# Kernel tuning notes

Hardware: AMD Instinct MI355X
Metric: run time of the kernel (lower is better)

The kernel has to match this reference:

```python
import jax, jax.numpy as jnp
import numpy as np

NA = 100000
NB = 100000
N_REL = 6
REL_SRC = ['A', 'B', 'A', 'B', 'A', 'B']
REL_DST = ['B', 'A', 'A', 'B', 'B', 'A']
N_NODES = {'A': NA, 'B': NB}
H_DIM, OUT_DIM, N_BASES, N_EDGES = 64, 16, 4, 500000


def setup_inputs() -> dict:
    key = jax.random.key(0)
    ks = jax.random.split(key, 16)
    inp = {
        'embed_A': jax.random.normal(ks[0], (NA, H_DIM), jnp.float32) * 0.1,
        'embed_B': jax.random.normal(ks[1], (NB, H_DIM), jnp.float32) * 0.1,
        'bias0': jnp.zeros((H_DIM,), jnp.float32),
        'w_comp1': jax.random.normal(ks[2], (N_REL, N_BASES), jnp.float32) * 0.5,
        'basis1': jax.random.normal(ks[3], (N_BASES, H_DIM, H_DIM), jnp.float32) * (1.0 / np.sqrt(H_DIM)),
        'bias1': jnp.zeros((H_DIM,), jnp.float32),
        'w_comp2': jax.random.normal(ks[4], (N_REL, N_BASES), jnp.float32) * 0.5,
        'basis2': jax.random.normal(ks[5], (N_BASES, H_DIM, OUT_DIM), jnp.float32) * (1.0 / np.sqrt(H_DIM)),
        'bias2': jnp.zeros((OUT_DIM,), jnp.float32),
    }
    for r in range(N_REL):
        inp[f'src_r{r}'] = jax.random.randint(ks[6 + r], (N_EDGES,), 0, N_NODES[REL_SRC[r]], jnp.int32)
        inp[f'dst_r{r}'] = jax.random.randint(jax.random.fold_in(ks[6 + r], 7), (N_EDGES,), 0, N_NODES[REL_DST[r]], jnp.int32)
    return inp


def _hetero_conv(h, W_rels, bias, edges, out_dim, activation):
    # h: dict ntype -> [N, d_in]; W_rels: None or [n_rel, d_in, d_out]
    out = {nt: jnp.zeros((N_NODES[nt], out_dim), h['A'].dtype) for nt in N_NODES}
    for r in range(N_REL):
        src_t, dst_t = REL_SRC[r], REL_DST[r]
        src, dst = edges[r]
        x = h[src_t] if W_rels is None else h[src_t] @ W_rels[r]  # [N_src, d_out]
        msg = x[src]  # gather: [E, d_out]
        n_dst = N_NODES[dst_t]
        agg = jax.ops.segment_sum(msg, dst, num_segments=n_dst)
        deg = jax.ops.segment_sum(jnp.ones((msg.shape[0],), msg.dtype), dst, num_segments=n_dst)
        out[dst_t] = out[dst_t] + agg / jnp.maximum(deg, 1.0)[:, None]  # norm='right'
    out = {nt: out[nt] + bias for nt in out}
    if activation is not None:
        out = {nt: activation(out[nt]) for nt in out}
    return out


def reference(embed_A, embed_B, bias0, w_comp1, basis1, bias1, w_comp2, basis2, bias2,
              src_r0, dst_r0, src_r1, dst_r1, src_r2, dst_r2,
              src_r3, dst_r3, src_r4, dst_r4, src_r5, dst_r5):
    edges = [(src_r0, dst_r0), (src_r1, dst_r1), (src_r2, dst_r2),
             (src_r3, dst_r3), (src_r4, dst_r4), (src_r5, dst_r5)]
    h = {'A': embed_A, 'B': embed_B}
    # layer 0: weight=False -> pure normalized aggregation + bias + relu
    h = _hetero_conv(h, None, bias0, edges, H_DIM, jax.nn.relu)
    # hidden layer with basis-decomposed weights
    W1 = jnp.einsum('rb,bio->rio', w_comp1, basis1)
    h = _hetero_conv(h, W1, bias1, edges, H_DIM, jax.nn.relu)
    # output layer, no activation
    W2 = jnp.einsum('rb,bio->rio', w_comp2, basis2)
    h = _hetero_conv(h, W2, bias2, edges, OUT_DIM, None)
    return h['A']  # logits for category node type
```

## Files before the change

### kernel.cpp

```cpp
#include <hip/hip_runtime.h>

#define NN 100000
#define EE 500000
#define DD 64
#define OD 16
#define NR 6
#define NBASE 4
#define BSH 10
#define NBK 98
#define SBLK 128
#define FLATN (NBK * SBLK)
#define STCAP 5632
#define DBIN 64
#define DBLK 128
#define FLAT2 (DBIN * DBLK)
#define NVR 8

struct Edges { const int* src[NR]; const int* dst[NR]; };

typedef __attribute__((ext_vector_type(8))) short bf16x8;
typedef __attribute__((ext_vector_type(4))) float f32x4;

__device__ __forceinline__ float bf2f(ushort u) {
    union { unsigned int i; float f; } v; v.i = ((unsigned int)u) << 16; return v.f;
}
__device__ __forceinline__ ushort f2bf(float f) {
    unsigned int x = __float_as_uint(f);
    unsigned int r = (x + 0x7fffu + ((x >> 16) & 1u)) >> 16;
    return (ushort)r;
}
__device__ __forceinline__ void bfpair(unsigned int u, float& lo, float& hi) {
    lo = __uint_as_float(u << 16);
    hi = __uint_as_float(u & 0xffff0000u);
}

__global__ __launch_bounds__(256) void build_w_kernel(
    const float* __restrict__ wc1, const float* __restrict__ b1,
    const float* __restrict__ wc2, const float* __restrict__ b2,
    ushort* __restrict__ Wp1, ushort* __restrict__ Wp2)
{
    int idx = blockIdx.x * blockDim.x + threadIdx.x;
    const int n1 = NR * DD * DD;
    const int n2 = NR * DD * OD;
    if (idx < n1) {
        int r = idx >> 12, rem = idx & 4095;
        int i = rem >> 6, o = rem & 63;
        float s = 0.f;
        #pragma unroll
        for (int b = 0; b < NBASE; ++b) s += wc1[r * NBASE + b] * b1[b * 4096 + rem];
        Wp1[(((size_t)(r * 8 + (i >> 3)) * 64 + o) << 3) + (i & 7)] = f2bf(s);
    } else if (idx < n1 + n2) {
        int j = idx - n1;
        int r = j >> 10, rem = j & 1023;
        int i = rem >> 4, o = rem & 15;
        float s = 0.f;
        #pragma unroll
        for (int b = 0; b < NBASE; ++b) s += wc2[r * NBASE + b] * b2[b * 1024 + rem];
        Wp2[(((size_t)(r * 8 + (i >> 3)) * 16 + o) << 3) + (i & 7)] = f2bf(s);
    }
}

__global__ __launch_bounds__(256) void cvt_kernel(
    const float* __restrict__ in, ushort* __restrict__ out, int n4)
{
    int i = blockIdx.x * 256 + threadIdx.x;
    if (i >= n4) return;
    float4 v = ((const float4*)in)[i];
    ushort4 o;
    o.x = f2bf(v.x); o.y = f2bf(v.y); o.z = f2bf(v.z); o.w = f2bf(v.w);
    ((ushort4*)out)[i] = o;
}

__global__ __launch_bounds__(256) void count_kernel(Edges ep, int* __restrict__ cnt_mat)
{
    __shared__ int h[NBK];
    int r = blockIdx.y, blk = blockIdx.x;
    const int* __restrict__ dst = ep.dst[r];
    const int chunk = (EE + SBLK - 1) / SBLK;
    int e0 = blk * chunk, e1 = min(e0 + chunk, EE);
    for (int i = threadIdx.x; i < NBK; i += 256) h[i] = 0;
    __syncthreads();
    for (int e = e0 + threadIdx.x; e < e1; e += 256)
        atomicAdd(&h[dst[e] >> BSH], 1);
    __syncthreads();
    for (int b = threadIdx.x; b < NBK; b += 256)
        cnt_mat[r * FLATN + b * SBLK + blk] = h[b];
}

__global__ __launch_bounds__(1024) void flat_scan_kernel(
    const int* __restrict__ cnt_mat, int* __restrict__ off_flat, int* __restrict__ bbase)
{
    __shared__ int wsum[16];
    const int TPE = 13;
    int r = blockIdx.x;
    int tid = threadIdx.x, lane = tid & 63, wid = tid >> 6;
    int base = tid * TPE;
    int v[TPE];
    int s = 0;
    #pragma unroll
    for (int j = 0; j < TPE; ++j) {
        int i = base + j;
        v[j] = (i < FLATN) ? cnt_mat[r * FLATN + i] : 0;
        s += v[j];
    }
    int si = s;
    #pragma unroll
    for (int off = 1; off < 64; off <<= 1) {
        int t = __shfl_up(si, off);
        if (lane >= off) si += t;
    }
    if (lane == 63) wsum[wid] = si;
    __syncthreads();
    if (wid == 0) {
        int ws = (lane < 16) ? wsum[lane] : 0;
        #pragma unroll
        for (int off = 1; off < 16; off <<= 1) {
            int t = __shfl_up(ws, off);
            if (lane >= off) ws += t;
        }
        if (lane < 16) wsum[lane] = ws;
    }
    __syncthreads();
    int texcl = (wid > 0 ? wsum[wid - 1] : 0) + (si - s);
    int part = 0;
    #pragma unroll
    for (int j = 0; j < TPE; ++j) {
        int i = base + j;
        if (i < FLATN) {
            int o = texcl + part;
            off_flat[r * FLATN + i] = o;
            if ((i & (SBLK - 1)) == 0) bbase[r * (NBK + 1) + (i >> 7)] = o;
        }
        part += v[j];
    }
    if (tid == 0) bbase[r * (NBK + 1) + NBK] = EE;
}

__global__ __launch_bounds__(256) void scatter2_kernel(
    Edges ep, const int* __restrict__ off_flat, unsigned int* __restrict__ ebuf)
{
    __shared__ int goff[NBK];
    __shared__ int lcnt[NBK];
    int r = blockIdx.y, blk = blockIdx.x;
    const int* __restrict__ src = ep.src[r];
    const int* __restrict__ dst = ep.dst[r];
    unsigned int* eb = ebuf + (size_t)r * EE;
    const int chunk = (EE + SBLK - 1) / SBLK;
    int e0 = blk * chunk, e1 = min(e0 + chunk, EE);
    if (threadIdx.x < NBK) {
        goff[threadIdx.x] = off_flat[r * FLATN + threadIdx.x * SBLK + blk];
        lcnt[threadIdx.x] = 0;
    }
    __syncthreads();
    for (int e = e0 + threadIdx.x; e < e1; e += 256) {
        int d = dst[e];
        int b = d >> BSH;
        int pos = goff[b] + atomicAdd(&lcnt[b], 1);
        eb[pos] = (unsigned int)src[e] | ((unsigned int)(d & 1023) << 17);
    }
}

__global__ __launch_bounds__(256) void csr_fine_kernel(
    const unsigned int* __restrict__ ebuf, const int* __restrict__ bbase,
    int* __restrict__ row_ptr, float* __restrict__ inv_deg, int* __restrict__ col_idx)
{
    __shared__ int nh[1024];
    __shared__ int nb[1024];
    __shared__ int wsum4[4];
    __shared__ int stage[STCAP];
    int r = blockIdx.y, b = blockIdx.x;
    int tid = threadIdx.x, lane = tid & 63, wid = tid >> 6;
    int gb = bbase[r * (NBK + 1) + b];
    int ge = bbase[r * (NBK + 1) + b + 1];
    int cnt = ge - gb;
    if (cnt > STCAP) cnt = STCAP;
    const unsigned int* eb = ebuf + (size_t)r * EE + gb;
    #pragma unroll
    for (int j = 0; j < 4; ++j) nh[tid * 4 + j] = 0;
    __syncthreads();
    for (int i = tid; i < cnt; i += 256)
        atomicAdd(&nh[(eb[i] >> 17) & 1023], 1);
    __syncthreads();
    int v0 = nh[tid * 4 + 0], v1 = nh[tid * 4 + 1], v2 = nh[tid * 4 + 2], v3 = nh[tid * 4 + 3];
    int s = v0 + v1 + v2 + v3;
    int si = s;
    #pragma unroll
    for (int off = 1; off < 64; off <<= 1) {
        int t = __shfl_up(si, off);
        if (lane >= off) si += t;
    }
    if (lane == 63) wsum4[wid] = si;
    __syncthreads();
    if (tid == 0) {
        int a = 0;
        #pragma unroll
        for (int k = 0; k < 4; ++k) { int t = wsum4[k]; wsum4[k] = a; a += t; }
    }
    __syncthreads();
    int texcl = wsum4[wid] + (si - s);
    int p0 = texcl, p1 = p0 + v0, p2 = p1 + v1, p3 = p2 + v2;
    nb[tid * 4 + 0] = p0; nb[tid * 4 + 1] = p1; nb[tid * 4 + 2] = p2; nb[tid * 4 + 3] = p3;
    {
        int node0 = b * 1024 + tid * 4;
        int pj[4] = { p0, p1, p2, p3 };
        int vj[4] = { v0, v1, v2, v3 };
        #pragma unroll
        for (int j = 0; j < 4; ++j) {
            int node = node0 + j;
            if (node < NN) {
                row_ptr[r * (NN + 1) + node] = gb + pj[j];
                inv_deg[r * NN + node] = 1.0f / (float)(vj[j] > 1 ? vj[j] : 1);
            }
        }
    }
    if (b == NBK - 1 && tid == 0) row_ptr[r * (NN + 1) + NN] = EE;
    #pragma unroll
    for (int j = 0; j < 4; ++j) nh[tid * 4 + j] = 0;
    __syncthreads();
    for (int i = tid; i < cnt; i += 256) {
        unsigned int w = eb[i];
        int loc = (w >> 17) & 1023;
        int pos = nb[loc] + atomicAdd(&nh[loc], 1);
        stage[pos] = (int)(w & 0x1ffffu);
    }
    __syncthreads();
    int* co = col_idx + (size_t)r * EE + gb;
    for (int i = tid; i < cnt; i += 256) co[i] = stage[i];
}

__device__ __forceinline__ int vdeg(int vr, int n, const int* __restrict__ rp)
{
    if (vr < 6) return rp[vr * (NN + 1) + n + 1] - rp[vr * (NN + 1) + n];
    if (vr == 6)
        return (rp[1 * (NN + 1) + n + 1] - rp[1 * (NN + 1) + n])
             + (rp[2 * (NN + 1) + n + 1] - rp[2 * (NN + 1) + n])
             + (rp[5 * (NN + 1) + n + 1] - rp[5 * (NN + 1) + n]);
    return (rp[0 * (NN + 1) + n + 1] - rp[0 * (NN + 1) + n])
         + (rp[3 * (NN + 1) + n + 1] - rp[3 * (NN + 1) + n])
         + (rp[4 * (NN + 1) + n + 1] - rp[4 * (NN + 1) + n]);
}

__global__ __launch_bounds__(256) void dhist_kernel(
    const int* __restrict__ row_ptr, int* __restrict__ cnt2)
{
    __shared__ int h[DBIN];
    int vr = blockIdx.y, blk = blockIdx.x;
    if (threadIdx.x < DBIN) h[threadIdx.x] = 0;
    __syncthreads();
    const int chunk = (NN + DBLK - 1) / DBLK;
    int n0 = blk * chunk, n1 = min(n0 + chunk, NN);
    for (int n = n0 + threadIdx.x; n < n1; n += 256)
        atomicAdd(&h[min(vdeg(vr, n, row_ptr), DBIN - 1)], 1);
    __syncthreads();
    if (threadIdx.x < DBIN) cnt2[vr * FLAT2 + threadIdx.x * DBLK + blk] = h[threadIdx.x];
}

__global__ __launch_bounds__(1024) void dscan_kernel(
    const int* __restrict__ cnt2, int* __restrict__ off2)
{
    __shared__ int wsum[16];
    const int TPE = 8;
    int vr = blockIdx.x;
    int tid = threadIdx.x, lane = tid & 63, wid = tid >> 6;
    int base = tid * TPE;
    int v[TPE];
    int s = 0;
    #pragma unroll
    for (int j = 0; j < TPE; ++j) { v[j] = cnt2[vr * FLAT2 + base + j]; s += v[j]; }
    int si = s;
    #pragma unroll
    for (int off = 1; off < 64; off <<= 1) {
        int t = __shfl_up(si, off);
        if (lane >= off) si += t;
    }
    if (lane == 63) wsum[wid] = si;
    __syncthreads();
    if (wid == 0) {
        int ws = (lane < 16) ? wsum[lane] : 0;
        #pragma unroll
        for (int off = 1; off < 16; off <<= 1) {
            int t = __shfl_up(ws, off);
            if (lane >= off) ws += t;
        }
        if (lane < 16) wsum[lane] = ws;
    }
    __syncthreads();
    int texcl = (wid > 0 ? wsum[wid - 1] : 0) + (si - s);
    int part = 0;
    #pragma unroll
    for (int j = 0; j < TPE; ++j) {
        off2[vr * FLAT2 + base + j] = texcl + part;
        part += v[j];
    }
}

__global__ __launch_bounds__(256) void dscatter_kernel(
    const int* __restrict__ row_ptr, const int* __restrict__ off2, int* __restrict__ perm)
{
    __shared__ int goff[DBIN];
    __shared__ int lcnt[DBIN];
    int vr = blockIdx.y, blk = blockIdx.x;
    if (threadIdx.x < DBIN) {
        goff[threadIdx.x] = off2[vr * FLAT2 + threadIdx.x * DBLK + blk];
        lcnt[threadIdx.x] = 0;
    }
    __syncthreads();
    const int chunk = (NN + DBLK - 1) / DBLK;
    int n0 = blk * chunk, n1 = min(n0 + chunk, NN);
    for (int n = n0 + threadIdx.x; n < n1; n += 256) {
        int b = min(vdeg(vr, n, row_ptr), DBIN - 1);
        int pos = goff[b] + atomicAdd(&lcnt[b], 1);
        perm[vr * NN + pos] = n;
    }
}

__global__ __launch_bounds__(256) void agg_kernel(
    const ushort* __restrict__ hA, const ushort* __restrict__ hB,
    const int* __restrict__ row_ptr, const int* __restrict__ col_idx,
    const float* __restrict__ inv_deg, const int* __restrict__ perm,
    ushort* __restrict__ zA, ushort* __restrict__ zB)
{
    const int relT[6]   = {1, 2, 5, 0, 3, 4};
    const int srcIsA[6] = {0, 1, 0, 1, 0, 1};
    int y = blockIdx.y;
    int r = relT[y];
    const ushort* F = srcIsA[y] ? hA : hB;
    ushort* z = (y < 3) ? zA : zB;
    int ks = (y < 3) ? y : y - 3;
    int tid = threadIdx.x;
    int wid = tid >> 6, lane = tid & 63;
    int grp = lane >> 3, sub = lane & 7;
    int idx = blockIdx.x * 32 + wid * 8 + grp;
    bool valid = (idx < NN);
    int n = valid ? perm[r * NN + idx] : 0;
    const int* rp = row_ptr + r * (NN + 1);
    const int* ci = col_idx + (size_t)r * EE;
    int s = valid ? rp[n] : 0;
    int e = valid ? rp[n + 1] : 0;
    float a0 = 0.f, a1 = 0.f, a2 = 0.f, a3 = 0.f, a4 = 0.f, a5 = 0.f, a6 = 0.f, a7 = 0.f;
    int t = s;
    for (; t + 2 <= e; t += 2) {
        int c0 = ci[t], c1 = ci[t + 1];
        int4 u = *(const int4*)(F + (size_t)c0 * DD + sub * 8);
        int4 w = *(const int4*)(F + (size_t)c1 * DD + sub * 8);
        float l, h;
        bfpair((unsigned int)u.x, l, h); a0 += l; a1 += h;
        bfpair((unsigned int)u.y, l, h); a2 += l; a3 += h;
        bfpair((unsigned int)u.z, l, h); a4 += l; a5 += h;
        bfpair((unsigned int)u.w, l, h); a6 += l; a7 += h;
        bfpair((unsigned int)w.x, l, h); a0 += l; a1 += h;
        bfpair((unsigned int)w.y, l, h); a2 += l; a3 += h;
        bfpair((unsigned int)w.z, l, h); a4 += l; a5 += h;
        bfpair((unsigned int)w.w, l, h); a6 += l; a7 += h;
    }
    if (t < e) {
        int c0 = ci[t];
        int4 u = *(const int4*)(F + (size_t)c0 * DD + sub * 8);
        float l, h;
        bfpair((unsigned int)u.x, l, h); a0 += l; a1 += h;
        bfpair((unsigned int)u.y, l, h); a2 += l; a3 += h;
        bfpair((unsigned int)u.z, l, h); a4 += l; a5 += h;
        bfpair((unsigned int)u.w, l, h); a6 += l; a7 += h;
    }
    if (valid) {
        float inv = inv_deg[r * NN + n];
        int4 o;
        o.x = (int)((unsigned int)f2bf(a0 * inv) | ((unsigned int)f2bf(a1 * inv) << 16));
        o.y = (int)((unsigned int)f2bf(a2 * inv) | ((unsigned int)f2bf(a3 * inv) << 16));
        o.z = (int)((unsigned int)f2bf(a4 * inv) | ((unsigned int)f2bf(a5 * inv) << 16));
        o.w = (int)((unsigned int)f2bf(a6 * inv) | ((unsigned int)f2bf(a7 * inv) << 16));
        *(int4*)(z + (size_t)n * 192 + ks * 64 + sub * 8) = o;
    }
}

__global__ __launch_bounds__(256) void layer0_kernel(
    const ushort* __restrict__ eA, const ushort* __restrict__ eB,
    const int* __restrict__ row_ptr, const int* __restrict__ col_idx,
    const float* __restrict__ inv_deg, const int* __restrict__ perm,
    const float* __restrict__ bias, ushort* __restrict__ hA, ushort* __restrict__ hB)
{
    int side = blockIdx.y;
    const int relT[2][3] = { {1, 2, 5}, {0, 3, 4} };
    int tid = threadIdx.x;
    int wid = tid >> 6, lane = tid & 63;
    int grp = lane >> 3, sub = lane & 7;
    int idx = blockIdx.x * 32 + wid * 8 + grp;
    bool valid = (idx < NN);
    int n = valid ? perm[(6 + side) * NN + idx] : 0;
    float acc[8];
    {
        float4 b0 = *(const float4*)(bias + sub * 8);
        float4 b1 = *(const float4*)(bias + sub * 8 + 4);
        acc[0] = b0.x; acc[1] = b0.y; acc[2] = b0.z; acc[3] = b0.w;
        acc[4] = b1.x; acc[5] = b1.y; acc[6] = b1.z; acc[7] = b1.w;
    }
    #pragma unroll
    for (int ks = 0; ks < 3; ++ks) {
        int r = relT[side][ks];
        const ushort* F = ((side == 0) == (ks == 1)) ? eA : eB;
        const int* rp = row_ptr + r * (NN + 1);
        const int* ci = col_idx + (size_t)r * EE;
        int s = valid ? rp[n] : 0;
        int e = valid ? rp[n + 1] : 0;
        float a0 = 0.f, a1 = 0.f, a2 = 0.f, a3 = 0.f, a4 = 0.f, a5 = 0.f, a6 = 0.f, a7 = 0.f;
        int t = s;
        for (; t + 2 <= e; t += 2) {
            int c0 = ci[t], c1 = ci[t + 1];
            int4 u = *(const int4*)(F + (size_t)c0 * DD + sub * 8);
            int4 w = *(const int4*)(F + (size_t)c1 * DD + sub * 8);
            float l, h;
            bfpair((unsigned int)u.x, l, h); a0 += l; a1 += h;
            bfpair((unsigned int)u.y, l, h); a2 += l; a3 += h;
            bfpair((unsigned int)u.z, l, h); a4 += l; a5 += h;
            bfpair((unsigned int)u.w, l, h); a6 += l; a7 += h;
            bfpair((unsigned int)w.x, l, h); a0 += l; a1 += h;
            bfpair((unsigned int)w.y, l, h); a2 += l; a3 += h;
            bfpair((unsigned int)w.z, l, h); a4 += l; a5 += h;
            bfpair((unsigned int)w.w, l, h); a6 += l; a7 += h;
        }
        if (t < e) {
            int c0 = ci[t];
            int4 u = *(const int4*)(F + (size_t)c0 * DD + sub * 8);
            float l, h;
            bfpair((unsigned int)u.x, l, h); a0 += l; a1 += h;
            bfpair((unsigned int)u.y, l, h); a2 += l; a3 += h;
            bfpair((unsigned int)u.z, l, h); a4 += l; a5 += h;
            bfpair((unsigned int)u.w, l, h); a6 += l; a7 += h;
        }
        float inv = valid ? inv_deg[r * NN + n] : 0.f;
        acc[0] += a0 * inv; acc[1] += a1 * inv; acc[2] += a2 * inv; acc[3] += a3 * inv;
        acc[4] += a4 * inv; acc[5] += a5 * inv; acc[6] += a6 * inv; acc[7] += a7 * inv;
    }
    if (valid) {
        ushort* h = side ? hB : hA;
        int4 o;
        o.x = (int)((unsigned int)f2bf(fmaxf(acc[0], 0.f)) | ((unsigned int)f2bf(fmaxf(acc[1], 0.f)) << 16));
        o.y = (int)((unsigned int)f2bf(fmaxf(acc[2], 0.f)) | ((unsigned int)f2bf(fmaxf(acc[3], 0.f)) << 16));
        o.z = (int)((unsigned int)f2bf(fmaxf(acc[4], 0.f)) | ((unsigned int)f2bf(fmaxf(acc[5], 0.f)) << 16));
        o.w = (int)((unsigned int)f2bf(fmaxf(acc[6], 0.f)) | ((unsigned int)f2bf(fmaxf(acc[7], 0.f)) << 16));
        *(int4*)(h + (size_t)n * DD + sub * 8) = o;
    }
}

__global__ __launch_bounds__(256) void gemm1_mfma_kernel(
    const ushort* __restrict__ A, const ushort* __restrict__ Wp,
    int r0, int r1, int r2, const float* __restrict__ bias, ushort* __restrict__ out)
{
    int tid = threadIdx.x;
    int wave = tid >> 6, lane = tid & 63;
    int q = lane & 15, p = lane >> 4;
    int n0 = blockIdx.x * 64 + wave * 16;
    int rr[3] = { r0, r1, r2 };
    f32x4 acc0 = {0.f, 0.f, 0.f, 0.f};
    f32x4 acc1 = {0.f, 0.f, 0.f, 0.f};
    f32x4 acc2 = {0.f, 0.f, 0.f, 0.f};
    f32x4 acc3 = {0.f, 0.f, 0.f, 0.f};
    const ushort* arow = A + (size_t)(n0 + q) * 192 + p * 8;
    #pragma unroll
    for (int ks = 0; ks < 3; ++ks) {
        int rel = rr[ks];
        #pragma unroll
        for (int t = 0; t < 2; ++t) {
            bf16x8 a = *(const bf16x8*)(arow + ks * 64 + t * 32);
            const ushort* wb = Wp + (((size_t)(rel * 8 + t * 4 + p) * 64 + q) << 3);
            bf16x8 b0 = *(const bf16x8*)(wb);
            bf16x8 b1 = *(const bf16x8*)(wb + 16 * 8);
            bf16x8 b2 = *(const bf16x8*)(wb + 32 * 8);
            bf16x8 b3 = *(const bf16x8*)(wb + 48 * 8);
            acc0 = __builtin_amdgcn_mfma_f32_16x16x32_bf16(a, b0, acc0, 0, 0, 0);
            acc1 = __builtin_amdgcn_mfma_f32_16x16x32_bf16(a, b1, acc1, 0, 0, 0);
            acc2 = __builtin_amdgcn_mfma_f32_16x16x32_bf16(a, b2, acc2, 0, 0, 0);
            acc3 = __builtin_amdgcn_mfma_f32_16x16x32_bf16(a, b3, acc3, 0, 0, 0);
        }
    }
    float bv0 = bias[q], bv1 = bias[16 + q], bv2 = bias[32 + q], bv3 = bias[48 + q];
    #pragma unroll
    for (int v = 0; v < 4; ++v) {
        int n = n0 + p * 4 + v;
        if (n < NN) {
            ushort* orow = out + (size_t)n * 64;
            orow[q]      = f2bf(fmaxf(acc0[v] + bv0, 0.f));
            orow[16 + q] = f2bf(fmaxf(acc1[v] + bv1, 0.f));
            orow[32 + q] = f2bf(fmaxf(acc2[v] + bv2, 0.f));
            orow[48 + q] = f2bf(fmaxf(acc3[v] + bv3, 0.f));
        }
    }
}

__global__ __launch_bounds__(256) void gemm2_mfma_kernel(
    const ushort* __restrict__ A, const ushort* __restrict__ Wp,
    int r0, int r1, int r2, const float* __restrict__ bias, float* __restrict__ out)
{
    int tid = threadIdx.x;
    int wave = tid >> 6, lane = tid & 63;
    int q = lane & 15, p = lane >> 4;
    int n0 = blockIdx.x * 64 + wave * 16;
    int rr[3] = { r0, r1, r2 };
    f32x4 acc = {0.f, 0.f, 0.f, 0.f};
    const ushort* arow = A + (size_t)(n0 + q) * 192 + p * 8;
    #pragma unroll
    for (int ks = 0; ks < 3; ++ks) {
        int rel = rr[ks];
        #pragma unroll
        for (int t = 0; t < 2; ++t) {
            bf16x8 a = *(const bf16x8*)(arow + ks * 64 + t * 32);
            bf16x8 b = *(const bf16x8*)(Wp + (((size_t)(rel * 8 + t * 4 + p) * 16 + q) << 3));
            acc = __builtin_amdgcn_mfma_f32_16x16x32_bf16(a, b, acc, 0, 0, 0);
        }
    }
    float bv = bias[q];
    #pragma unroll
    for (int v = 0; v < 4; ++v) {
        int n = n0 + p * 4 + v;
        if (n < NN) out[(size_t)n * 16 + q] = acc[v] + bv;
    }
}

extern "C" void kernel_launch(void* const* d_in, const int* in_sizes, int n_in,
                              void* d_out, int out_size, void* d_ws, size_t ws_size,
                              hipStream_t stream)
{
    const float* embA  = (const float*)d_in[0];
    const float* embB  = (const float*)d_in[1];
    const float* bias0 = (const float*)d_in[2];
    const float* wc1   = (const float*)d_in[3];
    const float* b1    = (const float*)d_in[4];
    const float* bias1 = (const float*)d_in[5];
    const float* wc2   = (const float*)d_in[6];
    const float* b2    = (const float*)d_in[7];
    const float* bias2 = (const float*)d_in[8];

    Edges ep;
    for (int r = 0; r < NR; ++r) {
        ep.src[r] = (const int*)d_in[9 + 2 * r];
        ep.dst[r] = (const int*)d_in[10 + 2 * r];
    }

    char* ws = (char*)d_ws;
    size_t off = 0;
    auto alloc = [&](size_t bytes) {
        void* p = ws + off;
        off = (off + bytes + 255) & ~(size_t)255;
        return p;
    };
    ushort* Wp1     = (ushort*)alloc((size_t)NR * 8 * 64 * 8 * 2);
    ushort* Wp2     = (ushort*)alloc((size_t)NR * 8 * 16 * 8 * 2);
    int*    cnt_mat = (int*)   alloc((size_t)NR * FLATN * 4);
    int*    off_fl  = (int*)   alloc((size_t)NR * FLATN * 4);
    int*    bbase   = (int*)   alloc((size_t)NR * (NBK + 1) * 4);
    int*    row_ptr = (int*)   alloc((size_t)NR * (NN + 1) * 4);
    float*  inv_deg = (float*) alloc((size_t)NR * NN * 4);
    int*    col_idx = (int*)   alloc((size_t)NR * EE * 4);
    int*    perm    = (int*)   alloc((size_t)NVR * NN * 4);
    ushort* zA      = (ushort*)alloc((size_t)NN * 192 * 2);
    ushort* zB      = (ushort*)alloc((size_t)NN * 192 * 2);
    ushort* h0A     = (ushort*)alloc((size_t)NN * DD * 2);
    ushort* h0B     = (ushort*)alloc((size_t)NN * DD * 2);
    ushort* h1A     = (ushort*)alloc((size_t)NN * DD * 2);
    ushort* h1B     = (ushort*)alloc((size_t)NN * DD * 2);
    (void)ws_size;

    unsigned int* ebuf   = (unsigned int*)zA;
    ushort*       embA16 = h1A;
    ushort*       embB16 = h1B;
    int*          cnt2   = cnt_mat;
    int*          off2   = off_fl;

    int nw = NR * DD * DD + NR * DD * OD;
    build_w_kernel<<<(nw + 255) / 256, 256, 0, stream>>>(wc1, b1, wc2, b2, Wp1, Wp2);
    cvt_kernel<<<(NN * DD / 4 + 255) / 256, 256, 0, stream>>>(embA, embA16, NN * DD / 4);
    cvt_kernel<<<(NN * DD / 4 + 255) / 256, 256, 0, stream>>>(embB, embB16, NN * DD / 4);

    count_kernel<<<dim3(SBLK, NR), 256, 0, stream>>>(ep, cnt_mat);
    flat_scan_kernel<<<NR, 1024, 0, stream>>>(cnt_mat, off_fl, bbase);
    scatter2_kernel<<<dim3(SBLK, NR), 256, 0, stream>>>(ep, off_fl, ebuf);
    csr_fine_kernel<<<dim3(NBK, NR), 256, 0, stream>>>(ebuf, bbase, row_ptr, inv_deg, col_idx);

    dhist_kernel<<<dim3(DBLK, NVR), 256, 0, stream>>>(row_ptr, cnt2);
    dscan_kernel<<<NVR, 1024, 0, stream>>>(cnt2, off2);
    dscatter_kernel<<<dim3(DBLK, NVR), 256, 0, stream>>>(row_ptr, off2, perm);

    int agx = (NN + 31) / 32;
    int ggrid = (NN + 63) / 64;

    layer0_kernel<<<dim3(agx, 2), 256, 0, stream>>>(
        embA16, embB16, row_ptr, col_idx, inv_deg, perm, bias0, h0A, h0B);

    agg_kernel<<<dim3(agx, 6), 256, 0, stream>>>(
        h0A, h0B, row_ptr, col_idx, inv_deg, perm, zA, zB);
    gemm1_mfma_kernel<<<ggrid, 256, 0, stream>>>(zA, Wp1, 1, 2, 5, bias1, h1A);
    gemm1_mfma_kernel<<<ggrid, 256, 0, stream>>>(zB, Wp1, 0, 3, 4, bias1, h1B);

    agg_kernel<<<dim3(agx, 3), 256, 0, stream>>>(
        h1A, h1B, row_ptr, col_idx, inv_deg, perm, zA, zB);
    gemm2_mfma_kernel<<<ggrid, 256, 0, stream>>>(zA, Wp2, 1, 2, 5, bias2, (float*)d_out);
}
```

Measured before the change: 310.7 us.

## Relabel nodes by degree-sorted order and fuse aggregation with MFMA GEMM per layer

After: 311.6 us. Within noise of the previous version (+0.3%).

```diff
diff --git a/kernel.cpp b/kernel.cpp
--- a/kernel.cpp
+++ b/kernel.cpp
@@ -12,9 +12,7 @@
 #define FLATN (NBK * SBLK)
 #define STCAP 5632
 #define DBIN 64
-#define DBLK 128
-#define FLAT2 (DBIN * DBLK)
-#define NVR 8
+#define LROW 100
 
 struct Edges { const int* src[NR]; const int* dst[NR]; };
 
@@ -58,17 +56,6 @@
         for (int b = 0; b < NBASE; ++b) s += wc2[r * NBASE + b] * b2[b * 1024 + rem];
         Wp2[(((size_t)(r * 8 + (i >> 3)) * 16 + o) << 3) + (i & 7)] = f2bf(s);
     }
-}
-
-__global__ __launch_bounds__(256) void cvt_kernel(
-    const float* __restrict__ in, ushort* __restrict__ out, int n4)
-{
-    int i = blockIdx.x * 256 + threadIdx.x;
-    if (i >= n4) return;
-    float4 v = ((const float4*)in)[i];
-    ushort4 o;
-    o.x = f2bf(v.x); o.y = f2bf(v.y); o.z = f2bf(v.z); o.w = f2bf(v.w);
-    ((ushort4*)out)[i] = o;
 }
 
 __global__ __launch_bounds__(256) void count_kernel(Edges ep, int* __restrict__ cnt_mat)
@@ -228,10 +215,9 @@
     for (int i = tid; i < cnt; i += 256) co[i] = stage[i];
 }
 
-__device__ __forceinline__ int vdeg(int vr, int n, const int* __restrict__ rp)
-{
-    if (vr < 6) return rp[vr * (NN + 1) + n + 1] - rp[vr * (NN + 1) + n];
-    if (vr == 6)
+__device__ __forceinline__ int sdeg(int vr, int n, const int* __restrict__ rp)
+{
+    if (vr == 0)
         return (rp[1 * (NN + 1) + n + 1] - rp[1 * (NN + 1) + n])
              + (rp[2 * (NN + 1) + n + 1] - rp[2 * (NN + 1) + n])
              + (rp[5 * (NN + 1) + n + 1] - rp[5 * (NN + 1) + n]);
@@ -240,137 +226,80 @@
          + (rp[4 * (NN + 1) + n + 1] - rp[4 * (NN + 1) + n]);
 }
 
-__global__ __launch_bounds__(256) void dhist_kernel(
-    const int* __restrict__ row_ptr, int* __restrict__ cnt2)
+__global__ __launch_bounds__(256) void bsort_kernel(
+    const int* __restrict__ row_ptr, int* __restrict__ perm, int* __restrict__ iperm)
 {
     __shared__ int h[DBIN];
-    int vr = blockIdx.y, blk = blockIdx.x;
-    if (threadIdx.x < DBIN) h[threadIdx.x] = 0;
-    __syncthreads();
-    const int chunk = (NN + DBLK - 1) / DBLK;
-    int n0 = blk * chunk, n1 = min(n0 + chunk, NN);
-    for (int n = n0 + threadIdx.x; n < n1; n += 256)
-        atomicAdd(&h[min(vdeg(vr, n, row_ptr), DBIN - 1)], 1);
-    __syncthreads();
-    if (threadIdx.x < DBIN) cnt2[vr * FLAT2 + threadIdx.x * DBLK + blk] = h[threadIdx.x];
-}
-
-__global__ __launch_bounds__(1024) void dscan_kernel(
-    const int* __restrict__ cnt2, int* __restrict__ off2)
-{
-    __shared__ int wsum[16];
-    const int TPE = 8;
-    int vr = blockIdx.x;
-    int tid = threadIdx.x, lane = tid & 63, wid = tid >> 6;
-    int base = tid * TPE;
-    int v[TPE];
-    int s = 0;
-    #pragma unroll
-    for (int j = 0; j < TPE; ++j) { v[j] = cnt2[vr * FLAT2 + base + j]; s += v[j]; }
-    int si = s;
-    #pragma unroll
-    for (int off = 1; off < 64; off <<= 1) {
-        int t = __shfl_up(si, off);
-        if (lane >= off) si += t;
-    }
-    if (lane == 63) wsum[wid] = si;
-    __syncthreads();
-    if (wid == 0) {
-        int ws = (lane < 16) ? wsum[lane] : 0;
-        #pragma unroll
-        for (int off = 1; off < 16; off <<= 1) {
-            int t = __shfl_up(ws, off);
-            if (lane >= off) ws += t;
-        }
-        if (lane < 16) wsum[lane] = ws;
-    }
-    __syncthreads();
-    int texcl = (wid > 0 ? wsum[wid - 1] : 0) + (si - s);
-    int part = 0;
-    #pragma unroll
-    for (int j = 0; j < TPE; ++j) {
-        off2[vr * FLAT2 + base + j] = texcl + part;
-        part += v[j];
-    }
-}
-
-__global__ __launch_bounds__(256) void dscatter_kernel(
-    const int* __restrict__ row_ptr, const int* __restrict__ off2, int* __restrict__ perm)
-{
-    __shared__ int goff[DBIN];
-    __shared__ int lcnt[DBIN];
-    int vr = blockIdx.y, blk = blockIdx.x;
-    if (threadIdx.x < DBIN) {
-        goff[threadIdx.x] = off2[vr * FLAT2 + threadIdx.x * DBLK + blk];
-        lcnt[threadIdx.x] = 0;
-    }
-    __syncthreads();
-    const int chunk = (NN + DBLK - 1) / DBLK;
-    int n0 = blk * chunk, n1 = min(n0 + chunk, NN);
-    for (int n = n0 + threadIdx.x; n < n1; n += 256) {
-        int b = min(vdeg(vr, n, row_ptr), DBIN - 1);
-        int pos = goff[b] + atomicAdd(&lcnt[b], 1);
-        perm[vr * NN + pos] = n;
-    }
-}
-
-__global__ __launch_bounds__(256) void agg_kernel(
-    const ushort* __restrict__ hA, const ushort* __restrict__ hB,
-    const int* __restrict__ row_ptr, const int* __restrict__ col_idx,
-    const float* __restrict__ inv_deg, const int* __restrict__ perm,
-    ushort* __restrict__ zA, ushort* __restrict__ zB)
-{
-    const int relT[6]   = {1, 2, 5, 0, 3, 4};
-    const int srcIsA[6] = {0, 1, 0, 1, 0, 1};
-    int y = blockIdx.y;
-    int r = relT[y];
-    const ushort* F = srcIsA[y] ? hA : hB;
-    ushort* z = (y < 3) ? zA : zB;
-    int ks = (y < 3) ? y : y - 3;
+    __shared__ int base_[DBIN];
+    int vr = blockIdx.y, b = blockIdx.x;
+    int n0 = b * 1024;
+    int cnt = min(1024, NN - n0);
     int tid = threadIdx.x;
-    int wid = tid >> 6, lane = tid & 63;
-    int grp = lane >> 3, sub = lane & 7;
-    int idx = blockIdx.x * 32 + wid * 8 + grp;
-    bool valid = (idx < NN);
-    int n = valid ? perm[r * NN + idx] : 0;
-    const int* rp = row_ptr + r * (NN + 1);
-    const int* ci = col_idx + (size_t)r * EE;
-    int s = valid ? rp[n] : 0;
-    int e = valid ? rp[n + 1] : 0;
-    float a0 = 0.f, a1 = 0.f, a2 = 0.f, a3 = 0.f, a4 = 0.f, a5 = 0.f, a6 = 0.f, a7 = 0.f;
-    int t = s;
-    for (; t + 2 <= e; t += 2) {
-        int c0 = ci[t], c1 = ci[t + 1];
-        int4 u = *(const int4*)(F + (size_t)c0 * DD + sub * 8);
-        int4 w = *(const int4*)(F + (size_t)c1 * DD + sub * 8);
-        float l, h;
-        bfpair((unsigned int)u.x, l, h); a0 += l; a1 += h;
-        bfpair((unsigned int)u.y, l, h); a2 += l; a3 += h;
-        bfpair((unsigned int)u.z, l, h); a4 += l; a5 += h;
-        bfpair((unsigned int)u.w, l, h); a6 += l; a7 += h;
-        bfpair((unsigned int)w.x, l, h); a0 += l; a1 += h;
-        bfpair((unsigned int)w.y, l, h); a2 += l; a3 += h;
-        bfpair((unsigned int)w.z, l, h); a4 += l; a5 += h;
-        bfpair((unsigned int)w.w, l, h); a6 += l; a7 += h;
-    }
-    if (t < e) {
-        int c0 = ci[t];
-        int4 u = *(const int4*)(F + (size_t)c0 * DD + sub * 8);
-        float l, h;
-        bfpair((unsigned int)u.x, l, h); a0 += l; a1 += h;
-        bfpair((unsigned int)u.y, l, h); a2 += l; a3 += h;
-        bfpair((unsigned int)u.z, l, h); a4 += l; a5 += h;
-        bfpair((unsigned int)u.w, l, h); a6 += l; a7 += h;
-    }
-    if (valid) {
-        float inv = inv_deg[r * NN + n];
-        int4 o;
-        o.x = (int)((unsigned int)f2bf(a0 * inv) | ((unsigned int)f2bf(a1 * inv) << 16));
-        o.y = (int)((unsigned int)f2bf(a2 * inv) | ((unsigned int)f2bf(a3 * inv) << 16));
-        o.z = (int)((unsigned int)f2bf(a4 * inv) | ((unsigned int)f2bf(a5 * inv) << 16));
-        o.w = (int)((unsigned int)f2bf(a6 * inv) | ((unsigned int)f2bf(a7 * inv) << 16));
-        *(int4*)(z + (size_t)n * 192 + ks * 64 + sub * 8) = o;
-    }
+    if (tid < DBIN) h[tid] = 0;
+    __syncthreads();
+    int bin[4];
+    #pragma unroll
+    for (int j = 0; j < 4; ++j) {
+        int i = tid + j * 256;
+        if (i < cnt) {
+            bin[j] = min(sdeg(vr, n0 + i, row_ptr), DBIN - 1);
+            atomicAdd(&h[bin[j]], 1);
+        } else bin[j] = -1;
+    }
+    __syncthreads();
+    if (tid < 64) {
+        int v = h[tid];
+        int s = v;
+        #pragma unroll
+        for (int off = 1; off < 64; off <<= 1) {
+            int t = __shfl_up(s, off);
+            if (tid >= off) s += t;
+        }
+        base_[tid] = s - v;
+        h[tid] = 0;
+    }
+    __syncthreads();
+    #pragma unroll
+    for (int j = 0; j < 4; ++j) {
+        if (bin[j] >= 0) {
+            int n = n0 + tid + j * 256;
+            int pos = n0 + base_[bin[j]] + atomicAdd(&h[bin[j]], 1);
+            perm[vr * NN + pos] = n;
+            iperm[vr * NN + n] = pos;
+        }
+    }
+}
+
+__global__ __launch_bounds__(256) void translate_kernel(
+    const int* __restrict__ iperm, int* __restrict__ col_idx)
+{
+    const int srcSide[NR] = {0, 1, 0, 1, 0, 1};
+    int r = blockIdx.y;
+    const int* ip = iperm + srcSide[r] * NN;
+    int* ci = col_idx + (size_t)r * EE;
+    for (int e = blockIdx.x * 256 + threadIdx.x; e < EE; e += gridDim.x * 256)
+        ci[e] = ip[ci[e]];
+}
+
+__global__ __launch_bounds__(256) void cvtp_kernel(
+    const float* __restrict__ inA, const float* __restrict__ inB,
+    const int* __restrict__ perm, ushort* __restrict__ outA, ushort* __restrict__ outB)
+{
+    int side = blockIdx.y;
+    int t = blockIdx.x * 256 + threadIdx.x;
+    if (t >= NN * 8) return;
+    int idx = t >> 3, j = t & 7;
+    int n = perm[side * NN + idx];
+    const float* in = side ? inB : inA;
+    ushort* out = side ? outB : outA;
+    float4 v0 = ((const float4*)in)[n * 16 + j * 2];
+    float4 v1 = ((const float4*)in)[n * 16 + j * 2 + 1];
+    int4 o;
+    o.x = (int)((unsigned int)f2bf(v0.x) | ((unsigned int)f2bf(v0.y) << 16));
+    o.y = (int)((unsigned int)f2bf(v0.z) | ((unsigned int)f2bf(v0.w) << 16));
+    o.z = (int)((unsigned int)f2bf(v1.x) | ((unsigned int)f2bf(v1.y) << 16));
+    o.w = (int)((unsigned int)f2bf(v1.z) | ((unsigned int)f2bf(v1.w) << 16));
+    *(int4*)(out + (size_t)idx * DD + j * 8) = o;
 }
 
 __global__ __launch_bounds__(256) void layer0_kernel(
@@ -386,7 +315,7 @@
     int grp = lane >> 3, sub = lane & 7;
     int idx = blockIdx.x * 32 + wid * 8 + grp;
     bool valid = (idx < NN);
-    int n = valid ? perm[(6 + side) * NN + idx] : 0;
+    int n = valid ? perm[side * NN + idx] : 0;
     float acc[8];
     {
         float4 b0 = *(const float4*)(bias + sub * 8);
@@ -419,8 +348,7 @@
             bfpair((unsigned int)w.w, l, h); a6 += l; a7 += h;
         }
         if (t < e) {
-            int c0 = ci[t];
-            int4 u = *(const int4*)(F + (size_t)c0 * DD + sub * 8);
+            int4 u = *(const int4*)(F + (size_t)ci[t] * DD + sub * 8);
             float l, h;
             bfpair((unsigned int)u.x, l, h); a0 += l; a1 += h;
             bfpair((unsigned int)u.y, l, h); a2 += l; a3 += h;
@@ -438,81 +366,187 @@
         o.y = (int)((unsigned int)f2bf(fmaxf(acc[2], 0.f)) | ((unsigned int)f2bf(fmaxf(acc[3], 0.f)) << 16));
         o.z = (int)((unsigned int)f2bf(fmaxf(acc[4], 0.f)) | ((unsigned int)f2bf(fmaxf(acc[5], 0.f)) << 16));
         o.w = (int)((unsigned int)f2bf(fmaxf(acc[6], 0.f)) | ((unsigned int)f2bf(fmaxf(acc[7], 0.f)) << 16));
-        *(int4*)(h + (size_t)n * DD + sub * 8) = o;
-    }
-}
-
-__global__ __launch_bounds__(256) void gemm1_mfma_kernel(
-    const ushort* __restrict__ A, const ushort* __restrict__ Wp,
-    int r0, int r1, int r2, const float* __restrict__ bias, ushort* __restrict__ out)
-{
+        *(int4*)(h + (size_t)idx * DD + sub * 8) = o;
+    }
+}
+
+__global__ __launch_bounds__(256) void layer1_fused_kernel(
+    const ushort* __restrict__ h0A, const ushort* __restrict__ h0B,
+    const int* __restrict__ row_ptr, const int* __restrict__ col_idx,
+    const float* __restrict__ inv_deg, const int* __restrict__ perm,
+    const ushort* __restrict__ Wp, const float* __restrict__ bias,
+    ushort* __restrict__ h1A, ushort* __restrict__ h1B)
+{
+    __shared__ unsigned int sZ[32 * LROW];
+    int side = blockIdx.y;
+    const int relT[2][3] = { {1, 2, 5}, {0, 3, 4} };
     int tid = threadIdx.x;
-    int wave = tid >> 6, lane = tid & 63;
+    int wid = tid >> 6, lane = tid & 63;
+    int grp = lane >> 3, sub = lane & 7;
+    int ln = wid * 8 + grp;
+    int idx0 = blockIdx.x * 32;
+    int idx = idx0 + ln;
+    bool valid = (idx < NN);
+    int n = valid ? perm[side * NN + idx] : 0;
+    #pragma unroll
+    for (int ks = 0; ks < 3; ++ks) {
+        int r = relT[side][ks];
+        const ushort* F = ((side == 0) == (ks == 1)) ? h0A : h0B;
+        const int* rp = row_ptr + r * (NN + 1);
+        const int* ci = col_idx + (size_t)r * EE;
+        int s = valid ? rp[n] : 0;
+        int e = valid ? rp[n + 1] : 0;
+        float a0 = 0.f, a1 = 0.f, a2 = 0.f, a3 = 0.f, a4 = 0.f, a5 = 0.f, a6 = 0.f, a7 = 0.f;
+        int t = s;
+        for (; t + 2 <= e; t += 2) {
+            int c0 = ci[t], c1 = ci[t + 1];
+            int4 u = *(const int4*)(F + (size_t)c0 * DD + sub * 8);
+            int4 w = *(const int4*)(F + (size_t)c1 * DD + sub * 8);
+            float l, h;
+            bfpair((unsigned int)u.x, l, h); a0 += l; a1 += h;
+            bfpair((unsigned int)u.y, l, h); a2 += l; a3 += h;
+            bfpair((unsigned int)u.z, l, h); a4 += l; a5 += h;
+            bfpair((unsigned int)u.w, l, h); a6 += l; a7 += h;
+            bfpair((unsigned int)w.x, l, h); a0 += l; a1 += h;
+            bfpair((unsigned int)w.y, l, h); a2 += l; a3 += h;
+            bfpair((unsigned int)w.z, l, h); a4 += l; a5 += h;
+            bfpair((unsigned int)w.w, l, h); a6 += l; a7 += h;
+        }
+        if (t < e) {
+            int4 u = *(const int4*)(F + (size_t)ci[t] * DD + sub * 8);
+            float l, h;
+            bfpair((unsigned int)u.x, l, h); a0 += l; a1 += h;
+            bfpair((unsigned int)u.y, l, h); a2 += l; a3 += h;
+            bfpair((unsigned int)u.z, l, h); a4 += l; a5 += h;
+            bfpair((unsigned int)u.w, l, h); a6 += l; a7 += h;
+        }
+        float inv = valid ? inv_deg[r * NN + n] : 0.f;
+        int4 o;
+        o.x = (int)((unsigned int)f2bf(a0 * inv) | ((unsigned int)f2bf(a1 * inv) << 16));
+        o.y = (int)((unsigned int)f2bf(a2 * inv) | ((unsigned int)f2bf(a3 * inv) << 16));
+        o.z = (int)((unsigned int)f2bf(a4 * inv) | ((unsigned int)f2bf(a5 * inv) << 16));
+        o.w = (int)((unsigned int)f2bf(a6 * inv) | ((unsigned int)f2bf(a7 * inv) << 16));
+        *(int4*)&sZ[ln * LROW + ks * 32 + sub * 4] = o;
+    }
+    __syncthreads();
     int q = lane & 15, p = lane >> 4;
-    int n0 = blockIdx.x * 64 + wave * 16;
-    int rr[3] = { r0, r1, r2 };
+    int base16 = (wid >> 1) * 16, cb = (wid & 1) * 32;
     f32x4 acc0 = {0.f, 0.f, 0.f, 0.f};
     f32x4 acc1 = {0.f, 0.f, 0.f, 0.f};
-    f32x4 acc2 = {0.f, 0.f, 0.f, 0.f};
-    f32x4 acc3 = {0.f, 0.f, 0.f, 0.f};
-    const ushort* arow = A + (size_t)(n0 + q) * 192 + p * 8;
     #pragma unroll
     for (int ks = 0; ks < 3; ++ks) {
-        int rel = rr[ks];
-        #pragma unroll
-        for (int t = 0; t < 2; ++t) {
-            bf16x8 a = *(const bf16x8*)(arow + ks * 64 + t * 32);
-            const ushort* wb = Wp + (((size_t)(rel * 8 + t * 4 + p) * 64 + q) << 3);
-            bf16x8 b0 = *(const bf16x8*)(wb);
+        int rel = relT[side][ks];
+        #pragma unroll
+        for (int tt = 0; tt < 2; ++tt) {
+            int4 t4 = *(const int4*)&sZ[(base16 + q) * LROW + (ks * 2 + tt) * 16 + p * 4];
+            bf16x8 a = *(const bf16x8*)&t4;
+            const ushort* wb = Wp + (((size_t)(rel * 8 + tt * 4 + p) * 64 + cb + q) << 3);
+            bf16x8 b0 = *(const bf16x8*)wb;
             bf16x8 b1 = *(const bf16x8*)(wb + 16 * 8);
-            bf16x8 b2 = *(const bf16x8*)(wb + 32 * 8);
-            bf16x8 b3 = *(const bf16x8*)(wb + 48 * 8);
             acc0 = __builtin_amdgcn_mfma_f32_16x16x32_bf16(a, b0, acc0, 0, 0, 0);
             acc1 = __builtin_amdgcn_mfma_f32_16x16x32_bf16(a, b1, acc1, 0, 0, 0);
-            acc2 = __builtin_amdgcn_mfma_f32_16x16x32_bf16(a, b2, acc2, 0, 0, 0);
-            acc3 = __builtin_amdgcn_mfma_f32_16x16x32_bf16(a, b3, acc3, 0, 0, 0);
-        }
-    }
-    float bv0 = bias[q], bv1 = bias[16 + q], bv2 = bias[32 + q], bv3 = bias[48 + q];
-    #pragma unroll
-    for (int v = 0; v < 4; ++v) {
-        int n = n0 + p * 4 + v;
-        if (n < NN) {
-            ushort* orow = out + (size_t)n * 64;
-            orow[q]      = f2bf(fmaxf(acc0[v] + bv0, 0.f));
-            orow[16 + q] = f2bf(fmaxf(acc1[v] + bv1, 0.f));
-            orow[32 + q] = f2bf(fmaxf(acc2[v] + bv2, 0.f));
-            orow[48 + q] = f2bf(fmaxf(acc3[v] + bv3, 0.f));
-        }
-    }
-}
-
-__global__ __launch_bounds__(256) void gemm2_mfma_kernel(
-    const ushort* __restrict__ A, const ushort* __restrict__ Wp,
-    int r0, int r1, int r2, const float* __restrict__ bias, float* __restrict__ out)
-{
+        }
+    }
+    __syncthreads();
+    ushort* sC = (ushort*)sZ;
+    {
+        float bv0 = bias[cb + q], bv1 = bias[cb + 16 + q];
+        #pragma unroll
+        for (int v = 0; v < 4; ++v) {
+            int row = base16 + p * 4 + v;
+            sC[row * 64 + cb + q]      = f2bf(fmaxf(acc0[v] + bv0, 0.f));
+            sC[row * 64 + cb + 16 + q] = f2bf(fmaxf(acc1[v] + bv1, 0.f));
+        }
+    }
+    __syncthreads();
+    ushort* out = side ? h1B : h1A;
+    int row = tid >> 3, c8 = (tid & 7) * 8;
+    if (idx0 + row < NN)
+        *(int4*)(out + (size_t)(idx0 + row) * DD + c8) = *(const int4*)(sC + row * 64 + c8);
+}
+
+__global__ __launch_bounds__(256) void layer2_fused_kernel(
+    const ushort* __restrict__ h1A, const ushort* __restrict__ h1B,
+    const int* __restrict__ row_ptr, const int* __restrict__ col_idx,
+    const float* __restrict__ inv_deg, const int* __restrict__ perm,
+    const ushort* __restrict__ Wp, const float* __restrict__ bias,
+    float* __restrict__ out)
+{
+    __shared__ unsigned int sZ[32 * LROW];
+    const int relT[3] = { 1, 2, 5 };
     int tid = threadIdx.x;
-    int wave = tid >> 6, lane = tid & 63;
-    int q = lane & 15, p = lane >> 4;
-    int n0 = blockIdx.x * 64 + wave * 16;
-    int rr[3] = { r0, r1, r2 };
-    f32x4 acc = {0.f, 0.f, 0.f, 0.f};
-    const ushort* arow = A + (size_t)(n0 + q) * 192 + p * 8;
+    int wid = tid >> 6, lane = tid & 63;
+    int grp = lane >> 3, sub = lane & 7;
+    int ln = wid * 8 + grp;
+    int idx0 = blockIdx.x * 32;
+    int idx = idx0 + ln;
+    bool valid = (idx < NN);
+    int n = valid ? perm[idx] : 0;
     #pragma unroll
     for (int ks = 0; ks < 3; ++ks) {
-        int rel = rr[ks];
-        #pragma unroll
-        for (int t = 0; t < 2; ++t) {
-            bf16x8 a = *(const bf16x8*)(arow + ks * 64 + t * 32);
-            bf16x8 b = *(const bf16x8*)(Wp + (((size_t)(rel * 8 + t * 4 + p) * 16 + q) << 3));
-            acc = __builtin_amdgcn_mfma_f32_16x16x32_bf16(a, b, acc, 0, 0, 0);
-        }
-    }
-    float bv = bias[q];
-    #pragma unroll
-    for (int v = 0; v < 4; ++v) {
-        int n = n0 + p * 4 + v;
-        if (n < NN) out[(size_t)n * 16 + q] = acc[v] + bv;
+        int r = relT[ks];
+        const ushort* F = (ks == 1) ? h1A : h1B;
+        const int* rp = row_ptr + r * (NN + 1);
+        const int* ci = col_idx + (size_t)r * EE;
+        int s = valid ? rp[n] : 0;
+        int e = valid ? rp[n + 1] : 0;
+        float a0 = 0.f, a1 = 0.f, a2 = 0.f, a3 = 0.f, a4 = 0.f, a5 = 0.f, a6 = 0.f, a7 = 0.f;
+        int t = s;
+        for (; t + 2 <= e; t += 2) {
+            int c0 = ci[t], c1 = ci[t + 1];
+            int4 u = *(const int4*)(F + (size_t)c0 * DD + sub * 8);
+            int4 w = *(const int4*)(F + (size_t)c1 * DD + sub * 8);
+            float l, h;
+            bfpair((unsigned int)u.x, l, h); a0 += l; a1 += h;
+            bfpair((unsigned int)u.y, l, h); a2 += l; a3 += h;
+            bfpair((unsigned int)u.z, l, h); a4 += l; a5 += h;
+            bfpair((unsigned int)u.w, l, h); a6 += l; a7 += h;
+            bfpair((unsigned int)w.x, l, h); a0 += l; a1 += h;
+            bfpair((unsigned int)w.y, l, h); a2 += l; a3 += h;
+            bfpair((unsigned int)w.z, l, h); a4 += l; a5 += h;
+            bfpair((unsigned int)w.w, l, h); a6 += l; a7 += h;
+        }
+        if (t < e) {
+            int4 u = *(const int4*)(F + (size_t)ci[t] * DD + sub * 8);
+            float l, h;
+            bfpair((unsigned int)u.x, l, h); a0 += l; a1 += h;
+            bfpair((unsigned int)u.y, l, h); a2 += l; a3 += h;
+            bfpair((unsigned int)u.z, l, h); a4 += l; a5 += h;
+            bfpair((unsigned int)u.w, l, h); a6 += l; a7 += h;
+        }
+        float inv = valid ? inv_deg[r * NN + n] : 0.f;
+        int4 o;
+        o.x = (int)((unsigned int)f2bf(a0 * inv) | ((unsigned int)f2bf(a1 * inv) << 16));
+        o.y = (int)((unsigned int)f2bf(a2 * inv) | ((unsigned int)f2bf(a3 * inv) << 16));
+        o.z = (int)((unsigned int)f2bf(a4 * inv) | ((unsigned int)f2bf(a5 * inv) << 16));
+        o.w = (int)((unsigned int)f2bf(a6 * inv) | ((unsigned int)f2bf(a7 * inv) << 16));
+        *(int4*)&sZ[ln * LROW + ks * 32 + sub * 4] = o;
+    }
+    __syncthreads();
+    if (wid < 2) {
+        int q = lane & 15, p = lane >> 4;
+        int base16 = wid * 16;
+        f32x4 acc = {0.f, 0.f, 0.f, 0.f};
+        #pragma unroll
+        for (int ks = 0; ks < 3; ++ks) {
+            int rel = relT[ks];
+            #pragma unroll
+            for (int tt = 0; tt < 2; ++tt) {
+                int4 t4 = *(const int4*)&sZ[(base16 + q) * LROW + (ks * 2 + tt) * 16 + p * 4];
+                bf16x8 a = *(const bf16x8*)&t4;
+                bf16x8 b = *(const bf16x8*)(Wp + (((size_t)(rel * 8 + tt * 4 + p) * 16 + q) << 3));
+                acc = __builtin_amdgcn_mfma_f32_16x16x32_bf16(a, b, acc, 0, 0, 0);
+            }
+        }
+        float bv = bias[q];
+        #pragma unroll
+        for (int v = 0; v < 4; ++v) {
+            int ridx = idx0 + base16 + p * 4 + v;
+            if (ridx < NN) {
+                int pn = perm[ridx];
+                out[(size_t)pn * OD + q] = acc[v] + bv;
+            }
+        }
     }
 }
 
@@ -551,47 +585,40 @@
     int*    row_ptr = (int*)   alloc((size_t)NR * (NN + 1) * 4);
     float*  inv_deg = (float*) alloc((size_t)NR * NN * 4);
     int*    col_idx = (int*)   alloc((size_t)NR * EE * 4);
-    int*    perm    = (int*)   alloc((size_t)NVR * NN * 4);
-    ushort* zA      = (ushort*)alloc((size_t)NN * 192 * 2);
-    ushort* zB      = (ushort*)alloc((size_t)NN * 192 * 2);
-    ushort* h0A     = (ushort*)alloc((size_t)NN * DD * 2);
-    ushort* h0B     = (ushort*)alloc((size_t)NN * DD * 2);
-    ushort* h1A     = (ushort*)alloc((size_t)NN * DD * 2);
-    ushort* h1B     = (ushort*)alloc((size_t)NN * DD * 2);
+    int*    perm    = (int*)   alloc((size_t)2 * NN * 4);
+    int*    iperm   = (int*)   alloc((size_t)2 * NN * 4);
+    ushort* reg1    = (ushort*)alloc((size_t)2 * NN * DD * 2);
+    ushort* h0pA    = (ushort*)alloc((size_t)NN * DD * 2);
+    ushort* h0pB    = (ushort*)alloc((size_t)NN * DD * 2);
     (void)ws_size;
 
-    unsigned int* ebuf   = (unsigned int*)zA;
-    ushort*       embA16 = h1A;
-    ushort*       embB16 = h1B;
-    int*          cnt2   = cnt_mat;
-    int*          off2   = off_fl;
+    unsigned int* ebuf  = (unsigned int*)reg1;
+    ushort*       embpA = reg1;
+    ushort*       embpB = reg1 + (size_t)NN * DD;
+    ushort*       h1pA  = reg1;
+    ushort*       h1pB  = reg1 + (size_t)NN * DD;
 
     int nw = NR * DD * DD + NR * DD * OD;
     build_w_kernel<<<(nw + 255) / 256, 256, 0, stream>>>(wc1, b1, wc2, b2, Wp1, Wp2);
-    cvt_kernel<<<(NN * DD / 4 + 255) / 256, 256, 0, stream>>>(embA, embA16, NN * DD / 4);
-    cvt_kernel<<<(NN * DD / 4 + 255) / 256, 256, 0, stream>>>(embB, embB16, NN * DD / 4);
 
     count_kernel<<<dim3(SBLK, NR), 256, 0, stream>>>(ep, cnt_mat);
     flat_scan_kernel<<<NR, 1024, 0, stream>>>(cnt_mat, off_fl, bbase);
     scatter2_kernel<<<dim3(SBLK, NR), 256, 0, stream>>>(ep, off_fl, ebuf);
     csr_fine_kernel<<<dim3(NBK, NR), 256, 0, stream>>>(ebuf, bbase, row_ptr, inv_deg, col_idx);
 
-    dhist_kernel<<<dim3(DBLK, NVR), 256, 0, stream>>>(row_ptr, cnt2);
-    dscan_kernel<<<NVR, 1024, 0, stream>>>(cnt2, off2);
-    dscatter_kernel<<<dim3(DBLK, NVR), 256, 0, stream>>>(row_ptr, off2, perm);
+    bsort_kernel<<<dim3(NBK, 2), 256, 0, stream>>>(row_ptr, perm, iperm);
+    translate_kernel<<<dim3(64, NR), 256, 0, stream>>>(iperm, col_idx);
+    cvtp_kernel<<<dim3((NN * 8 + 255) / 256, 2), 256, 0, stream>>>(
+        embA, embB, perm, embpA, embpB);
 
     int agx = (NN + 31) / 32;
-    int ggrid = (NN + 63) / 64;
 
     layer0_kernel<<<dim3(agx, 2), 256, 0, stream>>>(
-        embA16, embB16, row_ptr, col_idx, inv_deg, perm, bias0, h0A, h0B);
-
-    agg_kernel<<<dim3(agx, 6), 256, 0, stream>>>(
-        h0A, h0B, row_ptr, col_idx, inv_deg, perm, zA, zB);
-    gemm1_mfma_kernel<<<ggrid, 256, 0, stream>>>(zA, Wp1, 1, 2, 5, bias1, h1A);
-    gemm1_mfma_kernel<<<ggrid, 256, 0, stream>>>(zB, Wp1, 0, 3, 4, bias1, h1B);
-
-    agg_kernel<<<dim3(agx, 3), 256, 0, stream>>>(
-        h1A, h1B, row_ptr, col_idx, inv_deg, perm, zA, zB);
-    gemm2_mfma_kernel<<<ggrid, 256, 0, stream>>>(zA, Wp2, 1, 2, 5, bias2, (float*)d_out);
-}
+        embpA, embpB, row_ptr, col_idx, inv_deg, perm, bias0, h0pA, h0pB);
+
+    layer1_fused_kernel<<<dim3(agx, 2), 256, 0, stream>>>(
+        h0pA, h0pB, row_ptr, col_idx, inv_deg, perm, Wp1, bias1, h1pA, h1pB);
+
+    layer2_fused_kernel<<<agx, 256, 0, stream>>>(
+        h1pA, h1pB, row_ptr, col_idx, inv_deg, perm, Wp2, bias2, (float*)d_out);
+}
```
